# Optimization experiments

Measured on AMD Instinct MI355X. Metric: run time of the kernel, lower is better.

Reference implementation:

```python
import jax, jax.numpy as jnp
import numpy as np

N, M, KNN, KUP, POS_DIM = 15872, 35637, 5, 20, 32


def _pos_emb_table(n, d):
    # transformer-style sinusoidal table (matches PosEmb._define_pos_emb)
    pos = np.arange(n, dtype=np.float32)[:, None]
    i2 = np.arange(0, d, 2, dtype=np.float32)
    div = 10000.0 ** (i2 / d)
    pe = np.zeros((n, d), dtype=np.float32)
    pe[:, 0::2] = np.sin(pos / div)
    pe[:, 1::2] = np.cos(pos / div)
    return jnp.asarray(pe)


def _lrelu(x):
    return jnp.where(x > 0, x, 0.2 * x)


def _gather(x, idx):
    # x: [B,n,d], idx: [B,m,k] -> [B,m,k,d]
    return jax.vmap(lambda xb, ib: xb[ib])(x, idx)


def _knn_idx(x, k):
    # x: [B,n,d]; k nearest excluding self (torch knn drops column 0 of topk)
    xx = jnp.sum(x * x, axis=-1)
    neg = 2.0 * jnp.einsum('bnd,bmd->bnm', x, x) - xx[:, :, None] - xx[:, None, :]
    _, idx = jax.lax.top_k(neg, k + 1)
    return idx[..., 1:]


def _emb_block(feat, idx, ec_w1, ec_s1, ec_h1, ec_w2, ec_b2,
               w1, s1, h1, w2, s2, h2, w3, s3, h3, w4, b4):
    # get_graph_feature: [B,n,k,2*in] = cat(nbr - ctr, ctr)
    nbr = _gather(feat, idx)
    ctr = jnp.broadcast_to(feat[:, :, None, :], nbr.shape)
    e = jnp.concatenate([nbr - ctr, ctr], axis=-1)
    # edge_conv (1x1 conv2d = per-edge linear); BN folded into scale/shift (eval mode)
    e = _lrelu(jnp.einsum('bnkc,oc->bnko', e, ec_w1) * ec_s1 + ec_h1)
    e = jnp.einsum('bnkc,oc->bnko', e, ec_w2) + ec_b2
    f1 = jnp.max(e, axis=2)                                   # max over k neighbors -> [B,n,out]
    fmax = jnp.broadcast_to(jnp.max(f1, axis=1, keepdims=True), f1.shape)
    favg = jnp.broadcast_to(jnp.mean(f1, axis=1, keepdims=True), f1.shape)
    h = jnp.concatenate([feat, f1, fmax, favg], axis=-1)      # [B,n,3*out+in]
    # fc_out: 1x1 conv1d stack = per-point MLP with folded BN + LeakyReLU
    h = _lrelu(h @ w1.T * s1 + h1)
    h = _lrelu(h @ w2.T * s2 + h2)
    h = _lrelu(h @ w3.T * s3 + h3)
    return h @ w4.T + b4


def _forward(lx, ldx, pos_emb,
             b0_ec_w1, b0_ec_s1, b0_ec_h1, b0_ec_w2, b0_ec_b2,
             b0_fc_w1, b0_fc_s1, b0_fc_h1, b0_fc_w2, b0_fc_s2, b0_fc_h2,
             b0_fc_w3, b0_fc_s3, b0_fc_h3, b0_fc_w4, b0_fc_b4,
             b1_ec_w1, b1_ec_s1, b1_ec_h1, b1_ec_w2, b1_ec_b2,
             b1_fc_w1, b1_fc_s1, b1_fc_h1, b1_fc_w2, b1_fc_s2, b1_fc_h2,
             b1_fc_w3, b1_fc_s3, b1_fc_h3, b1_fc_w4, b1_fc_b4,
             up_inputs, up_w0, up_s0, up_h0, up_w_rest, up_s_rest, up_h_rest, up_wf, up_bf,
             dec_w0, dec_b0, dec_w1, dec_b1, dec_w2, dec_b2, dec_w3, dec_b3,
             dec_w4, dec_b4, dec_wf, dec_bf,
             idx0, up_idx):
    B = ldx.shape[0]
    feat_in = jnp.concatenate([ldx, jnp.broadcast_to(pos_emb[None], (B,) + pos_emb.shape)], axis=-1)  # [B,N,35]
    f0 = _emb_block(feat_in, idx0,
                    b0_ec_w1, b0_ec_s1, b0_ec_h1, b0_ec_w2, b0_ec_b2,
                    b0_fc_w1, b0_fc_s1, b0_fc_h1, b0_fc_w2, b0_fc_s2, b0_fc_h2,
                    b0_fc_w3, b0_fc_s3, b0_fc_h3, b0_fc_w4, b0_fc_b4)   # [B,N,64]
    idx1 = _knn_idx(f0, KNN)                                            # dynamic feature-space KNN
    f1 = _emb_block(f0, idx1,
                    b1_ec_w1, b1_ec_s1, b1_ec_h1, b1_ec_w2, b1_ec_b2,
                    b1_fc_w1, b1_fc_s1, b1_fc_h1, b1_fc_w2, b1_fc_s2, b1_fc_h2,
                    b1_fc_w3, b1_fc_s3, b1_fc_h3, b1_fc_w4, b1_fc_b4)   # [B,N,128]
    x_feat = jnp.concatenate([feat_in, f0, f1], axis=-1)                # [B,N,227]
    # Upscale: SIREN-activated 1x1-conv stack -> softmax interpolation weights over KUP lo-res nbrs
    h = jnp.sin(jnp.einsum('bmkc,oc->bmko', up_inputs[:B], up_w0) * up_s0 + up_h0)
    for i in range(up_w_rest.shape[0]):
        h = jnp.sin(jnp.einsum('bmkc,oc->bmko', h, up_w_rest[i]) * up_s_rest[i] + up_h_rest[i])
    logits = jnp.einsum('bmkc,oc->bmko', h, up_wf) + up_bf              # [B,M,KUP,1]
    w = jax.nn.softmax(logits, axis=2)
    grouped = _gather(x_feat, up_idx)                                   # [B,M,KUP,227]
    z = jnp.sum(w * grouped, axis=2)                                    # [B,M,227]
    # SIREN decoder: dims [227,256,128,64,32,16,3]; zip with 5 mods applies first 5 layers + head
    h = jnp.sin(30.0 * (z @ dec_w0.T + dec_b0))
    h = jnp.sin(h @ dec_w1.T + dec_b1)
    h = jnp.sin(h @ dec_w2.T + dec_b2)
    h = jnp.sin(h @ dec_w3.T + dec_b3)
    h = jnp.sin(h @ dec_w4.T + dec_b4)
    return h @ dec_wf.T + dec_bf                                        # [B,M,3]


def setup_inputs():
    key = jax.random.key(0)
    ks = iter(jax.random.split(key, 100))
    def rn(*s):
        return jax.random.normal(next(ks), s, jnp.float32) * 0.05
    def sc(*s):
        return jax.random.uniform(next(ks), s, jnp.float32, minval=0.5, maxval=1.5)
    inp = {}
    inp['lx'] = jax.random.normal(next(ks), (1, N, 3), jnp.float32)
    inp['ldx'] = jax.random.normal(next(ks), (1, N, 3), jnp.float32)
    inp['pos_emb'] = _pos_emb_table(N, POS_DIM)
    inp['idx0'] = jax.random.randint(next(ks), (1, N, KNN), 0, N - 1)
    # EmbModule 0: in=35, out=64
    inp['b0_ec_w1'], inp['b0_ec_s1'], inp['b0_ec_h1'] = rn(128, 70), sc(128), rn(128)
    inp['b0_ec_w2'], inp['b0_ec_b2'] = rn(64, 128), rn(64)
    inp['b0_fc_w1'], inp['b0_fc_s1'], inp['b0_fc_h1'] = rn(192, 227), sc(192), rn(192)
    inp['b0_fc_w2'], inp['b0_fc_s2'], inp['b0_fc_h2'] = rn(128, 192), sc(128), rn(128)
    inp['b0_fc_w3'], inp['b0_fc_s3'], inp['b0_fc_h3'] = rn(64, 128), sc(64), rn(64)
    inp['b0_fc_w4'], inp['b0_fc_b4'] = rn(64, 64), rn(64)
    # EmbModule 1: in=64, out=128
    inp['b1_ec_w1'], inp['b1_ec_s1'], inp['b1_ec_h1'] = rn(256, 128), sc(256), rn(256)
    inp['b1_ec_w2'], inp['b1_ec_b2'] = rn(128, 256), rn(128)
    inp['b1_fc_w1'], inp['b1_fc_s1'], inp['b1_fc_h1'] = rn(384, 448), sc(384), rn(384)
    inp['b1_fc_w2'], inp['b1_fc_s2'], inp['b1_fc_h2'] = rn(256, 384), sc(256), rn(256)
    inp['b1_fc_w3'], inp['b1_fc_s3'], inp['b1_fc_h3'] = rn(128, 256), sc(128), rn(128)
    inp['b1_fc_w4'], inp['b1_fc_b4'] = rn(128, 128), rn(128)
    inp['up_inputs'] = jax.random.uniform(next(ks), (1, M, KUP, 7), jnp.float32)
    inp['up_idx'] = jax.random.randint(next(ks), (1, M, KUP), 0, N - 1)
    inp['up_w0'], inp['up_s0'], inp['up_h0'] = rn(128, 7), sc(128), rn(128)
    inp['up_w_rest'], inp['up_s_rest'], inp['up_h_rest'] = rn(7, 128, 128), sc(7, 128), rn(7, 128)
    inp['up_wf'], inp['up_bf'] = rn(1, 128), rn(1)
    # SIREN decoder
    dd = [227, 256, 128, 64, 32, 16]
    for i in range(5):
        inp['dec_w%d' % i], inp['dec_b%d' % i] = rn(dd[i + 1], dd[i]), rn(dd[i + 1])
    inp['dec_wf'], inp['dec_bf'] = rn(3, 16), rn(3)
    return inp


def reference(lx, ldx, pos_emb, idx0,
              b0_ec_w1, b0_ec_s1, b0_ec_h1, b0_ec_w2, b0_ec_b2,
              b0_fc_w1, b0_fc_s1, b0_fc_h1, b0_fc_w2, b0_fc_s2, b0_fc_h2,
              b0_fc_w3, b0_fc_s3, b0_fc_h3, b0_fc_w4, b0_fc_b4,
              b1_ec_w1, b1_ec_s1, b1_ec_h1, b1_ec_w2, b1_ec_b2,
              b1_fc_w1, b1_fc_s1, b1_fc_h1, b1_fc_w2, b1_fc_s2, b1_fc_h2,
              b1_fc_w3, b1_fc_s3, b1_fc_h3, b1_fc_w4, b1_fc_b4,
              up_inputs, up_idx, up_w0, up_s0, up_h0,
              up_w_rest, up_s_rest, up_h_rest, up_wf, up_bf,
              dec_w0, dec_b0, dec_w1, dec_b1, dec_w2, dec_b2, dec_w3, dec_b3,
              dec_w4, dec_b4, dec_wf, dec_bf):
    return _forward(lx, ldx, pos_emb,
                    b0_ec_w1, b0_ec_s1, b0_ec_h1, b0_ec_w2, b0_ec_b2,
                    b0_fc_w1, b0_fc_s1, b0_fc_h1, b0_fc_w2, b0_fc_s2, b0_fc_h2,
                    b0_fc_w3, b0_fc_s3, b0_fc_h3, b0_fc_w4, b0_fc_b4,
                    b1_ec_w1, b1_ec_s1, b1_ec_h1, b1_ec_w2, b1_ec_b2,
                    b1_fc_w1, b1_fc_s1, b1_fc_h1, b1_fc_w2, b1_fc_s2, b1_fc_h2,
                    b1_fc_w3, b1_fc_s3, b1_fc_h3, b1_fc_w4, b1_fc_b4,
                    up_inputs, up_w0, up_s0, up_h0, up_w_rest, up_s_rest, up_h_rest, up_wf, up_bf,
                    dec_w0, dec_b0, dec_w1, dec_b1, dec_w2, dec_b2, dec_w3, dec_b3,
                    dec_w4, dec_b4, dec_wf, dec_bf,
                    idx0, up_idx)
```

## Files before the change

kernel.cpp:

```cpp
#include <hip/hip_runtime.h>
#include <hip/hip_bf16.h>
#include <math.h>

#define N_PTS 15872
#define M_PTS 35637
#define KNN_K 5
#define KUP   20
#define UP_ROWS (M_PTS * KUP)
#define NTILE (N_PTS/32)
#define N_EDGE (N_PTS*KNN_K)
#define CDIV(a,b) (((a)+(b)-1)/(b))

typedef __hip_bfloat16 bf16;
typedef unsigned int uint;
typedef unsigned short ushort_t;
__device__ __forceinline__ float b2f(bf16 x){ return __bfloat162float(x); }

__device__ __forceinline__ uint f2bf_bits(float x){
  uint u = __float_as_uint(x);
  return (u + 0x7FFFu + ((u>>16)&1u)) >> 16;
}

__device__ __forceinline__ ushort_t f2h_bits(float x){
  union { _Float16 h; ushort_t u; } c; c.h = (_Float16)x; return c.u;
}

typedef __attribute__((ext_vector_type(8))) short bf16x8;
typedef __attribute__((ext_vector_type(8))) _Float16 f16x8;
typedef __attribute__((ext_vector_type(2))) __fp16 fp16x2_t;
typedef __attribute__((ext_vector_type(16))) float f32x16;
union FragAB { bf16x8 v; uint u[4]; };
union FragB  { bf16x8 v; uint4 q; };
union FragH  { f16x8 v; uint4 q; _Float16 h[8]; };
union Acc16  { f32x16 v; float f[16]; };
union H2U    { fp16x2_t h; uint u; };

#define PSWAP(a,b) { \
  unsigned _ax = (unsigned)__shfl_xor((int)(a), 32, 64); \
  unsigned _bx = (unsigned)__shfl_xor((int)(b), 32, 64); \
  unsigned _na = hb2 ? _bx : (a); \
  unsigned _nb = hb2 ? (b) : _ax; \
  (a) = _na; (b) = _nb; }

__global__ void flag_k(const uint* __restrict__ pos_raw, int* __restrict__ flag){
  if (threadIdx.x == 0 && blockIdx.x == 0)
    flag[0] = (pos_raw[0] == 0x3F800000u) ? 1 : 0;
}

struct CvtTab { const void* src[52]; int start[52]; };
__global__ __launch_bounds__(256) void cvt_all_k(CvtTab tab, float* __restrict__ dst,
                                                 const int* __restrict__ flag, int total){
  int i = blockIdx.x*256 + threadIdx.x;
  if (i >= total) return;
  int s = 0;
#pragma unroll 1
  for (int k = 1; k < 52; k++) if (tab.start[k] <= i) s = k;
  int off = i - tab.start[s];
  float v = flag[0] ? b2f(((const bf16*)tab.src[s])[off]) : ((const float*)tab.src[s])[off];
  dst[i] = v;
}

__global__ void packfrag16_k(const float* __restrict__ w, const float* __restrict__ sr,
                             ushort_t* __restrict__ out, int n){
  int i = blockIdx.x*256 + threadIdx.x;
  if (i >= n) return;
  int j = i & 7;
  int lam = (i >> 3) & 63;
  int fg = i >> 9;
  int t = fg & 3, ks = (fg >> 2) & 1, Q = (fg >> 3) & 3, l = fg >> 5;
  int nn = t*32 + (lam & 31);
  int kk = Q*32 + ks*16 + (lam >> 5)*8 + j;
  float x = w[l*16384 + nn*128 + kk] * sr[l*128 + nn];
  out[i] = f2h_bits(x);
}

__global__ void packw_mfma_k(const float* __restrict__ w, ushort_t* __restrict__ whi,
                             ushort_t* __restrict__ wlo, int N, int K, int Kpad, int total){
  int i = blockIdx.x*256 + threadIdx.x;
  if (i >= total) return;
  int j = i & 7;
  int lane = (i >> 3) & 63;
  int fr = i >> 9;
  int nq = Kpad >> 5;
  int ks = fr & 1;
  int q  = (fr >> 1) % nq;
  int nt = (fr >> 1) / nq;
  int n = nt*32 + (lane & 31);
  int k = q*32 + ks*16 + (lane >> 5)*8 + j;
  float x = (n < N && k < K) ? w[(size_t)n*K + k] : 0.f;
  uint hb = f2bf_bits(x);
  uint lb = f2bf_bits(x - __uint_as_float(hb << 16));
  whi[i] = (ushort_t)hb;
  wlo[i] = (ushort_t)lb;
}

__global__ void packknn_k(const float* __restrict__ xf, const float* __restrict__ nr,
                          ushort_t* __restrict__ ahi, ushort_t* __restrict__ alo,
                          ushort_t* __restrict__ bhi, ushort_t* __restrict__ blo){
  int i = blockIdx.x*256 + threadIdx.x;
  if (i >= NTILE*5*64*8) return;
  int e = i & 7;
  int lane = (i >> 3) & 63;
  int rest = i >> 9;
  int kc = rest % 5, jt = rest / 5;
  int n = jt*32 + (lane & 31);
  int k = kc*16 + (lane >> 5)*8 + e;
  float f = (k < 64) ? xf[(size_t)n*227 + 35 + k] : 0.f;
  float av, bv;
  if (k < 64)      { av = 2.f*f;   bv = f; }
  else if (k == 64){ av = nr[n];   bv = -1.f; }
  else if (k == 65){ av = 1.f;     bv = -nr[n]; }
  else             { av = 0.f;     bv = 0.f; }
  uint ah = f2bf_bits(av); uint al = f2bf_bits(av - __uint_as_float(ah<<16));
  uint bh = f2bf_bits(bv); uint bl = f2bf_bits(bv - __uint_as_float(bh<<16));
  ahi[i] = (ushort_t)ah; alo[i] = (ushort_t)al;
  bhi[i] = (ushort_t)bh; blo[i] = (ushort_t)bl;
}

__global__ void fillmark_k(bf16* __restrict__ out, int n){
  int i = blockIdx.x*256 + threadIdx.x;
  if (i < n) out[i] = __float2bfloat16(12345.0f);
}

template<int EPI, int ACT>
__global__ __launch_bounds__(256) void gemm_k(
    const float* __restrict__ A, int lda,
    const float* __restrict__ W, int ldw,
    const float* __restrict__ scale, const float* __restrict__ shift,
    float gmul, float* __restrict__ C, int ldc,
    int M, int Nout, int K)
{
  __shared__ __align__(16) float As[16][64];
  __shared__ __align__(16) float Ws[16][64];
  const int tid = threadIdx.x;
  const int tx = tid & 15, ty = tid >> 4;
  const int bm = blockIdx.x * 64, bn = blockIdx.y * 64;
  const int ar = tid >> 2, ak = (tid & 3) * 4;
  float acc[4][4] = {};
  for (int k0 = 0; k0 < K; k0 += 16) {
    float a0=0.f,a1=0.f,a2=0.f,a3=0.f;
    int grow = bm + ar;
    if (grow < M) {
      const float* ap = A + (size_t)grow * lda + (k0 + ak);
      int rem = K - (k0 + ak);
      if (rem >= 4) { a0=ap[0]; a1=ap[1]; a2=ap[2]; a3=ap[3]; }
      else { if(rem>0)a0=ap[0]; if(rem>1)a1=ap[1]; if(rem>2)a2=ap[2]; }
    }
    float w0=0.f,w1=0.f,w2=0.f,w3=0.f;
    int gn = bn + ar;
    if (gn < Nout) {
      const float* wp = W + (size_t)gn * ldw + (k0 + ak);
      int rem = K - (k0 + ak);
      if (rem >= 4) { w0=wp[0]; w1=wp[1]; w2=wp[2]; w3=wp[3]; }
      else { if(rem>0)w0=wp[0]; if(rem>1)w1=wp[1]; if(rem>2)w2=wp[2]; }
    }
    __syncthreads();
    As[ak+0][ar]=a0; As[ak+1][ar]=a1; As[ak+2][ar]=a2; As[ak+3][ar]=a3;
    Ws[ak+0][ar]=w0; Ws[ak+1][ar]=w1; Ws[ak+2][ar]=w2; Ws[ak+3][ar]=w3;
    __syncthreads();
#pragma unroll
    for (int kk = 0; kk < 16; kk++) {
      float4 av = *reinterpret_cast<const float4*>(&As[kk][ty*4]);
      float4 wv = *reinterpret_cast<const float4*>(&Ws[kk][tx*4]);
      float aa[4] = {av.x,av.y,av.z,av.w};
      float ww[4] = {wv.x,wv.y,wv.z,wv.w};
#pragma unroll
      for (int i=0;i<4;i++)
#pragma unroll
        for (int j=0;j<4;j++) acc[i][j] += aa[i]*ww[j];
    }
  }
#pragma unroll
  for (int i=0;i<4;i++){
    int m = bm + ty*4 + i;
    if (m >= M) continue;
#pragma unroll
    for (int j=0;j<4;j++){
      int n = bn + tx*4 + j;
      if (n >= Nout) continue;
      float v = acc[i][j];
      if (EPI==0)      v = v * scale[n] + shift[n];
      else if (EPI==1) v = v + shift[n];
      else             v = (v + shift[n]) * gmul;
      if (ACT==1)      v = v > 0.f ? v : 0.2f*v;
      else if (ACT==2) v = sinf(v);
      C[(size_t)m*ldc + n] = v;
    }
  }
}

struct MLayer { int K, N, Kq, Nt, woff, soff, hoff, epi, act; float gmul; };
struct MCfg { MLayer L[6]; };

template<int NL, int OUTMODE>
__global__ __launch_bounds__(256) void mlp_fused_k(
    const float* __restrict__ A0, int lda0, int K0, int M,
    MCfg cfg,
    const ushort_t* __restrict__ wh, const ushort_t* __restrict__ wl,
    const float* __restrict__ wc,
    float* __restrict__ Cout, int ldc,
    void* __restrict__ oflg, const int* __restrict__ flag)
{
  __shared__ __align__(16) uint slab[64*256];
  const int tid = threadIdx.x;
  const int lane = tid & 63;
  const int wv = tid >> 6;
  const int np = lane & 31;
  const int hb2 = lane >> 5;
  const int rhalf = wv & 1, thalf = wv >> 1;
  const int rb = blockIdx.x * 64;
  const int row_l = rhalf*32 + np;

  for (int e = tid; e < 64*64; e += 256) {
    int r = e >> 6, g = e & 63;
    int gr = rb + r;
    uint p[4];
#pragma unroll
    for (int u=0;u<4;u++){
      int k = g*4+u;
      float f = (gr < M && k < K0) ? A0[(size_t)gr*lda0 + k] : 0.f;
      uint hb = f2bf_bits(f);
      uint lb = f2bf_bits(f - __uint_as_float(hb<<16));
      p[u] = (hb<<16) | lb;
    }
    *(uint4*)&slab[r*256 + (((g ^ r) & 63)<<2)] = make_uint4(p[0],p[1],p[2],p[3]);
  }
  __syncthreads();

#pragma unroll 1
  for (int l = 0; l < NL; l++){
    const int N = cfg.L[l].N, Kq = cfg.L[l].Kq, Nt = cfg.L[l].Nt;
    const int woff = cfg.L[l].woff, soff = cfg.L[l].soff, hoff = cfg.L[l].hoff;
    const int epi = cfg.L[l].epi, actf = cfg.L[l].act;
    const float gmul = cfg.L[l].gmul;
    Acc16 acc[4];
#pragma unroll
    for (int u=0;u<4;u++)
#pragma unroll
      for (int i=0;i<16;i++) acc[u].f[i] = 0.f;

#pragma unroll 1
    for (int q = 0; q < Kq; q++){
#pragma unroll
      for (int ks = 0; ks < 2; ks++){
        int g0 = (q*32 + ks*16 + hb2*8) >> 2;
        uint4 a0 = *(const uint4*)&slab[row_l*256 + ((((g0  ) ^ row_l) & 63)<<2)];
        uint4 a1 = *(const uint4*)&slab[row_l*256 + ((((g0+1) ^ row_l) & 63)<<2)];
        uint au[8] = {a0.x,a0.y,a0.z,a0.w,a1.x,a1.y,a1.z,a1.w};
        FragAB ah, al;
#pragma unroll
        for (int p=0;p<4;p++){
          ah.u[p] = (au[2*p]>>16)     | (au[2*p+1] & 0xFFFF0000u);
          al.u[p] = (au[2*p]&0xFFFFu) | (au[2*p+1]<<16);
        }
#pragma unroll
        for (int u=0;u<4;u++){
          int t = thalf + u*2;
          if (t < Nt){
            size_t fb = (size_t)woff + ((size_t)((t*Kq + q)*2 + ks))*512 + (size_t)lane*8;
            FragB bh, bl;
            bh.q = *(const uint4*)(wh + fb);
            bl.q = *(const uint4*)(wl + fb);
            acc[u].v = __builtin_amdgcn_mfma_f32_32x32x16_bf16(ah.v, bh.v, acc[u].v, 0,0,0);
            acc[u].v = __builtin_amdgcn_mfma_f32_32x32x16_bf16(al.v, bh.v, acc[u].v, 0,0,0);
            acc[u].v = __builtin_amdgcn_mfma_f32_32x32x16_bf16(ah.v, bl.v, acc[u].v, 0,0,0);
          }
        }
      }
    }
    __syncthreads();
#pragma unroll
    for (int u=0;u<4;u++){
      int t = thalf + u*2;
      if (t < Nt){
        int col = t*32 + np;
        if (col < N){
          float scv = (epi==0) ? wc[soff+col] : 0.f;
          float shv = wc[hoff+col];
#pragma unroll
          for (int reg=0;reg<16;reg++){
            int r32 = (reg&3) + 8*(reg>>2) + 4*hb2;
            float v = acc[u].f[reg];
            if (epi==0)      v = v*scv + shv;
            else if (epi==1) v = v + shv;
            else             v = (v + shv)*gmul;
            if (actf==1)      v = v > 0.f ? v : 0.2f*v;
            else if (actf==2) v = __sinf(v);
            if (l == NL-1){
              int gr = rb + rhalf*32 + r32;
              if (gr < M){
                if (OUTMODE==0) Cout[(size_t)gr*ldc + col] = v;
                else {
                  if (!(fabsf(v) < 1e30f)) v = 777.0f;
                  size_t oi = (size_t)gr*3 + col;
                  if (flag[0]) ((bf16*)oflg)[oi] = __float2bfloat16(v);
                  else         ((float*)oflg)[oi] = v;
                }
              }
            } else {
              int r = rhalf*32 + r32;
              uint hb = f2bf_bits(v);
              uint lb = f2bf_bits(v - __uint_as_float(hb<<16));
              slab[r*256 + ((((col>>2) ^ r) & 63)<<2) + (col&3)] = (hb<<16) | lb;
            }
          }
        }
      }
    }
    __syncthreads();
  }
}

#define INS5(tv, tj, v, j) \
  if ((v) > tv[4]){ tv[4]=(v); tj[4]=(j); \
    _Pragma("unroll") \
    for (int q=4;q>0;q--) \
      if (tv[q] > tv[q-1]){ float tf=tv[q-1]; tv[q-1]=tv[q]; tv[q]=tf; \
                            int ti=tj[q-1]; tj[q-1]=tj[q]; tj[q]=ti; } }

__global__ __launch_bounds__(256) void knn_mfma_k(
    const ushort_t* __restrict__ ahi, const ushort_t* __restrict__ alo,
    const ushort_t* __restrict__ bhi, const ushort_t* __restrict__ blo,
    int* __restrict__ out)
{
  __shared__ float mv[4][32][5];
  __shared__ int   mjj[4][32][5];
  const int tid = threadIdx.x;
  const int lane = tid & 63;
  const int wv = tid >> 6;
  const int np = lane & 31;
  const int hb2 = lane >> 5;
  const int it = blockIdx.x;
  const int ig = it*32 + np;

  FragB vh[5], vl[5];
  {
    size_t bb = (size_t)(it*5)*512 + (size_t)lane*8;
#pragma unroll
    for (int kc=0;kc<5;kc++){
      vh[kc].q = *(const uint4*)(bhi + bb + kc*512);
      vl[kc].q = *(const uint4*)(blo + bb + kc*512);
    }
  }

  float tv[5] = {-1e30f,-1e30f,-1e30f,-1e30f,-1e30f};
  int   tj[5] = {0,0,0,0,0};

  FragB uh[5], ul[5], nh[5], nl[5];
  {
    size_t ab = (size_t)(wv*5)*512 + (size_t)lane*8;
#pragma unroll
    for (int kc=0;kc<5;kc++){
      uh[kc].q = *(const uint4*)(ahi + ab + kc*512);
      ul[kc].q = *(const uint4*)(alo + ab + kc*512);
    }
  }

#pragma unroll 1
  for (int t = 0; t < NTILE/4; t++){
    int jt = wv + t*4;
    if (t+1 < NTILE/4){
      size_t an = (size_t)((jt+4)*5)*512 + (size_t)lane*8;
#pragma unroll
      for (int kc=0;kc<5;kc++){
        nh[kc].q = *(const uint4*)(ahi + an + kc*512);
        nl[kc].q = *(const uint4*)(alo + an + kc*512);
      }
    }
    Acc16 acc;
#pragma unroll
    for (int q=0;q<16;q++) acc.f[q] = 0.f;
#pragma unroll
    for (int kc=0;kc<5;kc++){
      acc.v = __builtin_amdgcn_mfma_f32_32x32x16_bf16(uh[kc].v, vh[kc].v, acc.v, 0,0,0);
      acc.v = __builtin_amdgcn_mfma_f32_32x32x16_bf16(ul[kc].v, vh[kc].v, acc.v, 0,0,0);
      acc.v = __builtin_amdgcn_mfma_f32_32x32x16_bf16(uh[kc].v, vl[kc].v, acc.v, 0,0,0);
    }
    int jb = jt*32 + 4*hb2;
#pragma unroll
    for (int reg=0;reg<16;reg++){
      int j = jb + (reg&3) + 8*(reg>>2);
      float v = acc.f[reg];
      if (j != ig) { INS5(tv, tj, v, j); }
    }
    if (t+1 < NTILE/4){
#pragma unroll
      for (int kc=0;kc<5;kc++){ uh[kc] = nh[kc]; ul[kc] = nl[kc]; }
    }
  }

#pragma unroll
  for (int s=0;s<5;s++){
    float ov = __shfl_xor(tv[s], 32, 64);
    int   oj = __shfl_xor(tj[s], 32, 64);
    INS5(tv, tj, ov, oj);
  }
  if (hb2 == 0){
#pragma unroll
    for (int s=0;s<5;s++){ mv[wv][np][s] = tv[s]; mjj[wv][np][s] = tj[s]; }
  }
  __syncthreads();
  if (tid < 32){
    float bv[5]; int bj[5];
#pragma unroll
    for (int s=0;s<5;s++){ bv[s] = mv[0][tid][s]; bj[s] = mjj[0][tid][s]; }
#pragma unroll
    for (int w=1;w<4;w++)
#pragma unroll
      for (int s=0;s<5;s++){
        float v = mv[w][tid][s]; int j = mjj[w][tid][s];
        INS5(bv, bj, v, j);
      }
    int gi = it*32 + tid;
#pragma unroll
    for (int s=0;s<5;s++) out[gi*KNN_K + s] = bj[s];
  }
}

__global__ __launch_bounds__(256) void siren_fused_k(
    const void* __restrict__ upin,
    const ushort_t* __restrict__ wf16,
    const float* __restrict__ W0c, const float* __restrict__ S0c, const float* __restrict__ H0c,
    const float* __restrict__ HRc,
    const float* __restrict__ WFc, const float* __restrict__ BFc,
    float* __restrict__ logits, const int* __restrict__ flag)
{
  __shared__ float intile[4*32*8];
  __shared__ __align__(16) float w0s[128*8];
  __shared__ __align__(16) float hrs[7*128];
  __shared__ __align__(16) float wfs[128];
  __shared__ float bfs[1];

  const int tid  = threadIdx.x;
  const int lane = tid & 63;
  const int wv   = tid >> 6;
  const int np   = lane & 31;
  const int hb2  = lane >> 5;
  const int rowbase = blockIdx.x * 128 + wv * 32;
  const int isbf = flag[0];
  float* intw = intile + wv*32*8;

  for (int e = tid; e < 128*7; e += 256){
    int c = e/7, k = e%7;
    w0s[c*8+k] = W0c[e]*S0c[c];
  }
  if (tid < 128) w0s[tid*8+7] = H0c[tid];
  for (int e = tid; e < 7*128; e += 256) hrs[e] = HRc[e];
  if (tid < 128) wfs[tid] = WFc[tid];
  if (tid == 0) bfs[0] = BFc[0];
  for (int e = lane; e < 32*7; e += 64) {
    int r = e/7, k = e%7;
    int gr = rowbase + r;
    float v = 0.f;
    if (gr < UP_ROWS)
      v = isbf ? b2f(((const bf16*)upin)[(size_t)gr*7+k]) : ((const float*)upin)[(size_t)gr*7+k];
    intw[r*8+k] = v;
  }
  __syncthreads();

  uint st0[16], st1[16];
  {
    float xin[7];
#pragma unroll
    for (int k=0;k<7;k++) xin[k] = intw[np*8+k];
#pragma unroll
    for (int g = 0; g < 16; g++){
      float xs[4];
#pragma unroll
      for (int j = 0; j < 4; j++){
        int c = g*8 + hb2*4 + j;
        const float4 wa = *(const float4*)&w0s[c*8];
        const float4 wb = *(const float4*)&w0s[c*8+4];
        float a = wb.w;
        a += xin[0]*wa.x; a += xin[1]*wa.y; a += xin[2]*wa.z; a += xin[3]*wa.w;
        a += xin[4]*wb.x; a += xin[5]*wb.y; a += xin[6]*wb.z;
        xs[j] = __sinf(a);
      }
      H2U u0,u1;
      u0.h = __builtin_amdgcn_cvt_pkrtz(xs[0],xs[1]);
      u1.h = __builtin_amdgcn_cvt_pkrtz(xs[2],xs[3]);
      st0[g] = u0.u; st1[g] = u1.u;
    }
  }

  FragH fr[8];
#pragma unroll
  for (int m = 0; m < 8; m++){
    uint a0 = st0[2*m], b0 = st0[2*m+1];
    uint a1 = st1[2*m], b1 = st1[2*m+1];
    PSWAP(a0,b0); PSWAP(a1,b1);
    fr[m].q = make_uint4(a0, a1, b0, b1);
  }

  uint nst0[16], nst1[16];
#pragma unroll 1
  for (int l = 0; l < 7; l++) {
#pragma unroll
    for (int tp = 0; tp < 2; tp++){
      Acc16 acc0, acc1;
#pragma unroll
      for (int i=0;i<16;i++){ acc0.f[i] = 0.f; acc1.f[i] = 0.f; }
#pragma unroll
      for (int m = 0; m < 8; m++){
        int fb = (((l*8 + m)*4 + tp*2) << 9) + lane*8;
        FragH bh0, bh1;
        bh0.q = *(const uint4*)(wf16 + fb);
        bh1.q = *(const uint4*)(wf16 + fb + 512);
        acc0.v = __builtin_amdgcn_mfma_f32_32x32x16_f16(bh0.v, fr[m].v, acc0.v, 0,0,0);
        acc1.v = __builtin_amdgcn_mfma_f32_32x32x16_f16(bh1.v, fr[m].v, acc1.v, 0,0,0);
      }
#pragma unroll
      for (int rg = 0; rg < 4; rg++){
        int g0 = (tp*2+0)*4 + rg;
        const float4 b0v = *(const float4*)&hrs[l*128 + g0*8 + hb2*4];
        float x0 = __sinf(acc0.f[rg*4+0] + b0v.x);
        float x1 = __sinf(acc0.f[rg*4+1] + b0v.y);
        float x2 = __sinf(acc0.f[rg*4+2] + b0v.z);
        float x3 = __sinf(acc0.f[rg*4+3] + b0v.w);
        H2U u0,u1;
        u0.h = __builtin_amdgcn_cvt_pkrtz(x0,x1);
        u1.h = __builtin_amdgcn_cvt_pkrtz(x2,x3);
        nst0[g0] = u0.u; nst1[g0] = u1.u;

        int g1 = (tp*2+1)*4 + rg;
        const float4 b1v = *(const float4*)&hrs[l*128 + g1*8 + hb2*4];
        float y0 = __sinf(acc1.f[rg*4+0] + b1v.x);
        float y1 = __sinf(acc1.f[rg*4+1] + b1v.y);
        float y2 = __sinf(acc1.f[rg*4+2] + b1v.z);
        float y3 = __sinf(acc1.f[rg*4+3] + b1v.w);
        H2U v0,v1;
        v0.h = __builtin_amdgcn_cvt_pkrtz(y0,y1);
        v1.h = __builtin_amdgcn_cvt_pkrtz(y2,y3);
        nst0[g1] = v0.u; nst1[g1] = v1.u;
      }
    }
    if (l < 6){
#pragma unroll
      for (int m = 0; m < 8; m++){
        uint a0 = nst0[2*m], b0 = nst0[2*m+1];
        uint a1 = nst1[2*m], b1 = nst1[2*m+1];
        PSWAP(a0,b0); PSWAP(a1,b1);
        fr[m].q = make_uint4(a0, a1, b0, b1);
      }
    }
  }

  {
    float a = 0.f;
#pragma unroll
    for (int g = 0; g < 16; g++){
      const float4 w4 = *(const float4*)&wfs[g*8 + hb2*4];
      H2U u0,u1; u0.u = nst0[g]; u1.u = nst1[g];
      a += (float)u0.h.x*w4.x + (float)u0.h.y*w4.y
         + (float)u1.h.x*w4.z + (float)u1.h.y*w4.w;
    }
    a += __shfl_xor(a, 32, 64);
    int gr = rowbase + np;
    if (hb2 == 0 && gr < UP_ROWS) logits[gr] = a + bfs[0];
  }
}

__global__ void featin_k(const void* __restrict__ ldx, const void* __restrict__ pos,
                         float* __restrict__ xf, const int* __restrict__ flag){
  int i = blockIdx.x*256 + threadIdx.x;
  if (i >= N_PTS*35) return;
  int n = i / 35, c = i % 35;
  float v;
  if (flag[0]) {
    v = (c < 3) ? b2f(((const bf16*)ldx)[n*3+c]) : b2f(((const bf16*)pos)[n*32 + (c-3)]);
  } else {
    v = (c < 3) ? ((const float*)ldx)[n*3+c] : ((const float*)pos)[n*32 + (c-3)];
  }
  xf[(size_t)n*227 + c] = v;
}

__global__ void gather_e_k(const float* __restrict__ xf, int coff, int CIN,
                           const int* __restrict__ idx, float* __restrict__ e,
                           int n0, int np){
  int W2 = 2*CIN;
  int i = blockIdx.x*256 + threadIdx.x;
  if (i >= np*KNN_K*W2) return;
  int c = i % W2; int ek = i / W2;
  int nl = ek / KNN_K, k = ek % KNN_K;
  int n = n0 + nl;
  int j = idx[n*KNN_K + k];
  float out;
  if (c < CIN) out = xf[(size_t)j*227 + coff + c] - xf[(size_t)n*227 + coff + c];
  else         out = xf[(size_t)n*227 + coff + (c-CIN)];
  e[(size_t)ek*W2 + c] = out;
}

__global__ void kmax_k(const float* __restrict__ e2, int C, float* __restrict__ f1,
                       int n0, int np){
  int i = blockIdx.x*256 + threadIdx.x;
  if (i >= np*C) return;
  int nl = i / C, c = i % C;
  float v = -1e30f;
  for (int k=0;k<KNN_K;k++) v = fmaxf(v, e2[((size_t)nl*KNN_K+k)*C + c]);
  f1[(size_t)(n0+nl)*C + c] = v;
}

template<int C>
__global__ __launch_bounds__(256) void reduce1_k(const float* __restrict__ X, int n,
                                                 float* __restrict__ pmax, float* __restrict__ psum){
  const int tid = threadIdx.x;
  const int c = tid % C;
  const int r0 = tid / C;
  const int TPR = 256 / C;
  float vmax = -1e30f, vsum = 0.f;
  for (int row = blockIdx.x * TPR + r0; row < n; row += gridDim.x * TPR) {
    float v = X[(size_t)row * C + c];
    vmax = fmaxf(vmax, v); vsum += v;
  }
  __shared__ float smax[256], ssum[256];
  smax[tid]=vmax; ssum[tid]=vsum;
  __syncthreads();
  if (tid < C) {
    for (int q=1;q<TPR;q++){ vmax=fmaxf(vmax, smax[q*C+c]); vsum += ssum[q*C+c]; }
    pmax[blockIdx.x*C + c] = vmax; psum[blockIdx.x*C + c] = vsum;
  }
}

template<int C>
__global__ void reduce2_k(const float* __restrict__ pmax, const float* __restrict__ psum,
                          int nblk, float invn, float* __restrict__ fmaxo, float* __restrict__ favgo){
  int c = threadIdx.x; if (c >= C) return;
  float vmax=-1e30f, vsum=0.f;
  for (int b=0;b<nblk;b++){ vmax=fmaxf(vmax,pmax[b*C+c]); vsum+=psum[b*C+c]; }
  fmaxo[c]=vmax; favgo[c]=vsum*invn;
}

__global__ void concat_k(const float* __restrict__ xf, int coff, int CF,
                         const float* __restrict__ f1, int C,
                         const float* __restrict__ fmax, const float* __restrict__ favg,
                         float* __restrict__ h, int n0, int np){
  int W = CF + 3*C;
  int i = blockIdx.x*256 + threadIdx.x;
  if (i >= np*W) return;
  int nl = i / W, c = i % W;
  int n = n0 + nl;
  float v;
  if (c < CF)          v = xf[(size_t)n*227 + coff + c];
  else if (c < CF+C)   v = f1[(size_t)n*C + (c-CF)];
  else if (c < CF+2*C) v = fmax[c-CF-C];
  else                 v = favg[c-CF-2*C];
  h[(size_t)nl*W + c] = v;
}

__global__ void norms_k(const float* __restrict__ xf, float* __restrict__ nr){
  int n = blockIdx.x*256 + threadIdx.x;
  if (n >= N_PTS) return;
  const float* p = xf + (size_t)n*227 + 35;
  float s = 0.f;
  for (int d=0;d<64;d++) s += p[d]*p[d];
  nr[n] = s;
}

__global__ __launch_bounds__(64) void softgather_k(const float* __restrict__ logits,
                                                   const int* __restrict__ up_idx,
                                                   const float* __restrict__ xf,
                                                   float* __restrict__ z){
  __shared__ float lw[KUP]; __shared__ int li[KUP];
  int m = blockIdx.x;
  int tid = threadIdx.x;
  if (tid < KUP){ lw[tid] = logits[(size_t)m*KUP + tid]; li[tid] = up_idx[(size_t)m*KUP + tid]; }
  __syncthreads();
  float mx = -1e30f;
  for (int k=0;k<KUP;k++) mx = fmaxf(mx, lw[k]);
  __syncthreads();
  if (tid < KUP) lw[tid] = expf(lw[tid]-mx);
  __syncthreads();
  float s = 0.f;
  for (int k=0;k<KUP;k++) s += lw[k];
  float inv = 1.f/s;
  for (int c = tid; c < 227; c += 64){
    float acc = 0.f;
    for (int k=0;k<KUP;k++) acc += lw[k] * xf[(size_t)li[k]*227 + c];
    z[(size_t)m*227 + c] = acc*inv;
  }
}

extern "C" void kernel_launch(void* const* d_in, const int* in_sizes, int n_in,
                              void* d_out, int out_size, void* d_ws, size_t ws_size,
                              hipStream_t stream) {
  const int *idx0  = (const int*)d_in[3];
  const int *upidx = (const int*)d_in[37];

  float* ws = (float*)d_ws;
  float* x_feat = ws;
  float* f1b    = ws + 3602944;
  float* pmax   = ws + 5634560;
  float* psum   = ws + 5667328;
  float* fmaxv  = ws + 5700096;
  float* favgv  = ws + 5700224;
  int*   flag   = (int*)(ws + 5700352);
  int*   idx1   = (int*)(ws + 5700368);
  float* nrm    = ws + 5779728;
  float* logits = ws + 5795600;
  float* wcvt   = ws + 6508352;
  float* S      = ws + 7214400;
  ushort_t* whi  = (ushort_t*)(S + 9662464);
  ushort_t* wlo  = whi + 114688;
  ushort_t* gwhi = wlo + 114688;
  ushort_t* gwlo = gwhi + 331776;

  const size_t NEED = (size_t)(7214400 + 9662464) * 4
                    + (size_t)(114688*2 + 331776*2) * 2;
  if (ws_size < NEED) {
    fillmark_k<<<CDIV(out_size,256),256,0,stream>>>((bf16*)d_out, out_size);
    return;
  }

  flag_k<<<1,64,0,stream>>>((const uint*)d_in[2], flag);
  CvtTab tab;
  int wcoff = 0, seg = 0;
  auto CVT = [&](int i, int n)->const float* {
    tab.src[seg] = d_in[i]; tab.start[seg] = wcoff; seg++;
    const float* p = wcvt + wcoff; wcoff += n;
    return p;
  };
  const float *E0W1=CVT(4,8960),  *E0S1=CVT(5,128),  *E0H1=CVT(6,128),
              *E0W2=CVT(7,8192),  *E0B2=CVT(8,64);
  const float *F0W1=CVT(9,43584), *F0S1=CVT(10,192), *F0H1=CVT(11,192),
              *F0W2=CVT(12,24576),*F0S2=CVT(13,128), *F0H2=CVT(14,128),
              *F0W3=CVT(15,8192), *F0S3=CVT(16,64),  *F0H3=CVT(17,64),
              *F0W4=CVT(18,4096), *F0B4=CVT(19,64);
  const float *E1W1=CVT(20,32768),*E1S1=CVT(21,256), *E1H1=CVT(22,256),
              *E1W2=CVT(23,32768),*E1B2=CVT(24,128);
  const float *F1W1=CVT(25,172032),*F1S1=CVT(26,384),*F1H1=CVT(27,384),
              *F1W2=CVT(28,98304),*F1S2=CVT(29,256), *F1H2=CVT(30,256),
              *F1W3=CVT(31,32768),*F1S3=CVT(32,128), *F1H3=CVT(33,128),
              *F1W4=CVT(34,16384),*F1B4=CVT(35,128);
  const float *UPW0=CVT(38,896),  *UPS0=CVT(39,128), *UPH0=CVT(40,128),
              *UPWR=CVT(41,114688),*UPSR=CVT(42,896),*UPHR=CVT(43,896),
              *UPWF=CVT(44,128),  *UPBF=CVT(45,1);
  const float *DW0=CVT(46,58112), *DB0=CVT(47,256),
              *DW1=CVT(48,32768), *DB1=CVT(49,128),
              *DW2=CVT(50,8192),  *DB2=CVT(51,64),
              *DW3=CVT(52,2048),  *DB3=CVT(53,32),
              *DW4=CVT(54,512),   *DB4=CVT(55,16),
              *DWF=CVT(56,48),    *DBF=CVT(57,3);
  cvt_all_k<<<CDIV(wcoff,256),256,0,stream>>>(tab, wcvt, flag, wcoff);

  packfrag16_k<<<CDIV(114688,256),256,0,stream>>>(UPWR, UPSR, whi, 114688);

  int offs[16]; const float* srcs[16]; int Ns[16], Ks[16], Kps[16];
  {
    int o = 0, q = 0;
    auto REG = [&](const float* s, int N, int K, int Kpad){
      srcs[q]=s; Ns[q]=N; Ks[q]=K; Kps[q]=Kpad; offs[q]=o;
      o += CDIV(N,32)*32*Kpad; q++;
    };
    REG(F0W1,192,227,256); REG(F0W2,128,192,192); REG(F0W3,64,128,128); REG(F0W4,64,64,64);
    REG(DW0,256,227,256);  REG(DW1,128,256,256);  REG(DW2,64,128,128);
    REG(DW3,32,64,64);     REG(DW4,16,32,32);     REG(DWF,3,16,32);
    REG(E0W1,128,70,96);   REG(E0W2,64,128,128);
    REG(E1W1,256,128,128); REG(E1W2,128,256,256);
    REG(F1W3,128,256,256); REG(F1W4,128,128,128);
  }
  for (int q = 0; q < 16; q++){
    int total = CDIV(Ns[q],32)*32*Kps[q];
    packw_mfma_k<<<CDIV(total,256),256,0,stream>>>(srcs[q], gwhi+offs[q], gwlo+offs[q],
                                                   Ns[q], Ks[q], Kps[q], total);
  }

  auto OFF = [&](const float* p){ return (int)(p - wcvt); };
  MCfg cfc0{};
  cfc0.L[0] = {227,192,8,6, offs[0], OFF(F0S1), OFF(F0H1), 0,1, 0.f};
  cfc0.L[1] = {192,128,6,4, offs[1], OFF(F0S2), OFF(F0H2), 0,1, 0.f};
  cfc0.L[2] = {128, 64,4,2, offs[2], OFF(F0S3), OFF(F0H3), 0,1, 0.f};
  cfc0.L[3] = { 64, 64,2,2, offs[3], 0,         OFF(F0B4), 1,0, 0.f};
  MCfg cdec{};
  cdec.L[0] = {227,256,8,8, offs[4], 0, OFF(DB0), 2,2, 30.f};
  cdec.L[1] = {256,128,8,4, offs[5], 0, OFF(DB1), 1,2, 0.f};
  cdec.L[2] = {128, 64,4,2, offs[6], 0, OFF(DB2), 1,2, 0.f};
  cdec.L[3] = { 64, 32,2,1, offs[7], 0, OFF(DB3), 1,2, 0.f};
  cdec.L[4] = { 32, 16,1,1, offs[8], 0, OFF(DB4), 1,2, 0.f};
  cdec.L[5] = { 16,  3,1,1, offs[9], 0, OFF(DBF), 1,0, 0.f};
  MCfg ce0{};
  ce0.L[0] = { 70,128,3,4, offs[10], OFF(E0S1), OFF(E0H1), 0,1, 0.f};
  ce0.L[1] = {128, 64,4,2, offs[11], 0,         OFF(E0B2), 1,0, 0.f};
  MCfg ce1{};
  ce1.L[0] = {128,256,4,8, offs[12], OFF(E1S1), OFF(E1H1), 0,1, 0.f};
  ce1.L[1] = {256,128,8,4, offs[13], 0,         OFF(E1B2), 1,0, 0.f};
  MCfg cf1t{};
  cf1t.L[0] = {256,128,8,4, offs[14], OFF(F1S3), OFF(F1H3), 0,1, 0.f};
  cf1t.L[1] = {128,128,4,4, offs[15], 0,         OFF(F1B4), 1,0, 0.f};

  const float invN = 1.f/(float)N_PTS;
  const int CHN = 8192;

  featin_k<<<CDIV(N_PTS*35,256),256,0,stream>>>(d_in[1], d_in[2], x_feat, flag);

  {
    const int P0 = N_PTS/2;
    for (int n0 = 0; n0 < N_PTS; n0 += P0) {
      int ne = P0 * KNN_K;
      float* eA   = S;
      float* eOut = S + 2777600;
      gather_e_k<<<CDIV(ne*70,256),256,0,stream>>>(x_feat, 0, 35, idx0, eA, n0, P0);
      mlp_fused_k<2,0><<<CDIV(ne,64),256,0,stream>>>(
          eA,70,70,ne, ce0, gwhi,gwlo,wcvt, eOut,64, nullptr, flag);
      kmax_k<<<CDIV(P0*64,256),256,0,stream>>>(eOut, 64, f1b, n0, P0);
    }
  }
  reduce1_k<64><<<256,256,0,stream>>>(f1b, N_PTS, pmax, psum);
  reduce2_k<64><<<1,64,0,stream>>>(pmax, psum, 256, invN, fmaxv, favgv);
  {
    float* h = S;
    concat_k<<<CDIV(N_PTS*227,256),256,0,stream>>>(x_feat,0,35, f1b,64, fmaxv,favgv, h, 0, N_PTS);
    mlp_fused_k<4,0><<<CDIV(N_PTS,64),256,0,stream>>>(
        h,227,227,N_PTS, cfc0, gwhi,gwlo,wcvt, x_feat+35,227, nullptr, flag);
  }

  norms_k<<<CDIV(N_PTS,256),256,0,stream>>>(x_feat, nrm);
  {
    const int PLANE = NTILE*5*64*8;
    ushort_t* ajhi = (ushort_t*)S;
    ushort_t* ajlo = ajhi + PLANE;
    ushort_t* bihi = ajlo + PLANE;
    ushort_t* bilo = bihi + PLANE;
    packknn_k<<<CDIV(PLANE,256),256,0,stream>>>(x_feat, nrm, ajhi, ajlo, bihi, bilo);
    knn_mfma_k<<<NTILE,256,0,stream>>>(ajhi, ajlo, bihi, bilo, idx1);
  }

  {
    const int P1 = 5952;
    for (int n0 = 0; n0 < N_PTS; n0 += P1) {
      int np = N_PTS - n0; if (np > P1) np = P1;
      int ne = np * KNN_K;
      float* eA   = S;
      float* eOut = S + 3809280;
      gather_e_k<<<CDIV(ne*128,256),256,0,stream>>>(x_feat, 35, 64, idx1, eA, n0, np);
      mlp_fused_k<2,0><<<CDIV(ne,64),256,0,stream>>>(
          eA,128,128,ne, ce1, gwhi,gwlo,wcvt, eOut,128, nullptr, flag);
      kmax_k<<<CDIV(np*128,256),256,0,stream>>>(eOut, 128, f1b, n0, np);
    }
  }
  reduce1_k<128><<<256,256,0,stream>>>(f1b, N_PTS, pmax, psum);
  reduce2_k<128><<<1,128,0,stream>>>(pmax, psum, 256, invN, fmaxv, favgv);
  for (int n0 = 0; n0 < N_PTS; n0 += CHN) {
    int np = N_PTS - n0; if (np > CHN) np = CHN;
    float* h  = S;
    float* a1 = S + 3670016;
    int gx = CDIV(np,64);
    concat_k<<<CDIV(np*448,256),256,0,stream>>>(x_feat,35,64, f1b,128, fmaxv,favgv, h, n0, np);
    gemm_k<0,1><<<dim3(gx,6),256,0,stream>>>(h,448,  F1W1,448, F1S1,F1H1,0.f, a1,384, np,384,448);
    gemm_k<0,1><<<dim3(gx,4),256,0,stream>>>(a1,384, F1W2,384, F1S2,F1H2,0.f, h,256,  np,256,384);
    mlp_fused_k<2,0><<<gx,256,0,stream>>>(
        h,256,256,np, cf1t, gwhi,gwlo,wcvt, x_feat+(size_t)n0*227+99,227, nullptr, flag);
  }

  siren_fused_k<<<CDIV(UP_ROWS,128),256,0,stream>>>(
      d_in[36], whi, UPW0, UPS0, UPH0, UPHR, UPWF, UPBF, logits, flag);
  float* zbuf = S;
  softgather_k<<<M_PTS,64,0,stream>>>(logits, upidx, x_feat, zbuf);

  mlp_fused_k<6,1><<<CDIV(M_PTS,64),256,0,stream>>>(
      zbuf,227,227,M_PTS, cdec, gwhi,gwlo,wcvt, nullptr,0, d_out, flag);
}
```

Measured before the change: 1.994 ms.

## Fold broadcast global max/avg features into first-layer bias; drop SIREN shuffle swaps

The global max and mean features are identical for every point, so their contribution through the first fc layer is precomputed once per block as a per-output bias (W·v·scale + shift). This shrinks the concat and the first GEMM K dimension from 227 to 99 and from 448 to 192, removing redundant matmul work and memory traffic. It also re-packs the SIREN fp16 weight fragments so the per-layer cross-lane shuffle swaps are no longer needed. The trade-off is extra small kernels and reliance on the new fragment packing being consistent with the MFMA operand layout.

```diff
diff --git a/kernel.cpp b/kernel.cpp
--- a/kernel.cpp
+++ b/kernel.cpp
@@ -35,13 +35,6 @@
 union Acc16  { f32x16 v; float f[16]; };
 union H2U    { fp16x2_t h; uint u; };
 
-#define PSWAP(a,b) { \
-  unsigned _ax = (unsigned)__shfl_xor((int)(a), 32, 64); \
-  unsigned _bx = (unsigned)__shfl_xor((int)(b), 32, 64); \
-  unsigned _na = hb2 ? _bx : (a); \
-  unsigned _nb = hb2 ? (b) : _ax; \
-  (a) = _na; (b) = _nb; }
-
 __global__ void flag_k(const uint* __restrict__ pos_raw, int* __restrict__ flag){
   if (threadIdx.x == 0 && blockIdx.x == 0)
     flag[0] = (pos_raw[0] == 0x3F800000u) ? 1 : 0;
@@ -69,13 +62,14 @@
   int fg = i >> 9;
   int t = fg & 3, ks = (fg >> 2) & 1, Q = (fg >> 3) & 3, l = fg >> 5;
   int nn = t*32 + (lam & 31);
-  int kk = Q*32 + ks*16 + (lam >> 5)*8 + j;
+  int kk = Q*32 + ks*16 + ((j>>2)<<3) + ((lam>>5)<<2) + (j&3);
   float x = w[l*16384 + nn*128 + kk] * sr[l*128 + nn];
   out[i] = f2h_bits(x);
 }
 
 __global__ void packw_mfma_k(const float* __restrict__ w, ushort_t* __restrict__ whi,
-                             ushort_t* __restrict__ wlo, int N, int K, int Kpad, int total){
+                             ushort_t* __restrict__ wlo, int N, int K, int ldk,
+                             int Kpad, int total){
   int i = blockIdx.x*256 + threadIdx.x;
   if (i >= total) return;
   int j = i & 7;
@@ -87,7 +81,7 @@
   int nt = (fr >> 1) / nq;
   int n = nt*32 + (lane & 31);
   int k = q*32 + ks*16 + (lane >> 5)*8 + j;
-  float x = (n < N && k < K) ? w[(size_t)n*K + k] : 0.f;
+  float x = (n < N && k < K) ? w[(size_t)n*ldk + k] : 0.f;
   uint hb = f2bf_bits(x);
   uint lb = f2bf_bits(x - __uint_as_float(hb << 16));
   whi[i] = (ushort_t)hb;
@@ -120,6 +114,20 @@
 __global__ void fillmark_k(bf16* __restrict__ out, int n){
   int i = blockIdx.x*256 + threadIdx.x;
   if (i < n) out[i] = __float2bfloat16(12345.0f);
+}
+
+__global__ void foldshift_k(const float* __restrict__ W, int ldw,
+                            int off1, int C1, const float* __restrict__ v1,
+                            int off2, int C2, const float* __restrict__ v2,
+                            const float* __restrict__ scale, const float* __restrict__ shift,
+                            float* __restrict__ out, int N){
+  int n = blockIdx.x*256 + threadIdx.x;
+  if (n >= N) return;
+  const float* wr = W + (size_t)n*ldw;
+  float s = 0.f;
+  for (int j=0;j<C1;j++) s += wr[off1+j]*v1[j];
+  for (int j=0;j<C2;j++) s += wr[off2+j]*v2[j];
+  out[n] = s*scale[n] + shift[n];
 }
 
 template<int EPI, int ACT>
@@ -485,12 +493,8 @@
 
   FragH fr[8];
 #pragma unroll
-  for (int m = 0; m < 8; m++){
-    uint a0 = st0[2*m], b0 = st0[2*m+1];
-    uint a1 = st1[2*m], b1 = st1[2*m+1];
-    PSWAP(a0,b0); PSWAP(a1,b1);
-    fr[m].q = make_uint4(a0, a1, b0, b1);
-  }
+  for (int m = 0; m < 8; m++)
+    fr[m].q = make_uint4(st0[2*m], st1[2*m], st0[2*m+1], st1[2*m+1]);
 
   uint nst0[16], nst1[16];
 #pragma unroll 1
@@ -536,12 +540,8 @@
     }
     if (l < 6){
 #pragma unroll
-      for (int m = 0; m < 8; m++){
-        uint a0 = nst0[2*m], b0 = nst0[2*m+1];
-        uint a1 = nst1[2*m], b1 = nst1[2*m+1];
-        PSWAP(a0,b0); PSWAP(a1,b1);
-        fr[m].q = make_uint4(a0, a1, b0, b1);
-      }
+      for (int m = 0; m < 8; m++)
+        fr[m].q = make_uint4(nst0[2*m], nst1[2*m], nst0[2*m+1], nst1[2*m+1]);
     }
   }
 
@@ -644,6 +644,18 @@
   else if (c < CF+C)   v = f1[(size_t)n*C + (c-CF)];
   else if (c < CF+2*C) v = fmax[c-CF-C];
   else                 v = favg[c-CF-2*C];
+  h[(size_t)nl*W + c] = v;
+}
+
+__global__ void concat2_k(const float* __restrict__ xf, int coff, int CF,
+                          const float* __restrict__ f1, int C,
+                          float* __restrict__ h, int n0, int np){
+  int W = CF + C;
+  int i = blockIdx.x*256 + threadIdx.x;
+  if (i >= np*W) return;
+  int nl = i / W, c = i % W;
+  int n = n0 + nl;
+  float v = (c < CF) ? xf[(size_t)n*227 + coff + c] : f1[(size_t)n*C + (c-CF)];
   h[(size_t)nl*W + c] = v;
 }
 
@@ -699,6 +711,8 @@
   float* logits = ws + 5795600;
   float* wcvt   = ws + 6508352;
   float* S      = ws + 7214400;
+  float* fold0  = S + 9500000;
+  float* fold1  = S + 9500192;
   ushort_t* whi  = (ushort_t*)(S + 9662464);
   ushort_t* wlo  = whi + 114688;
   ushort_t* gwhi = wlo + 114688;
@@ -744,29 +758,31 @@
 
   packfrag16_k<<<CDIV(114688,256),256,0,stream>>>(UPWR, UPSR, whi, 114688);
 
-  int offs[16]; const float* srcs[16]; int Ns[16], Ks[16], Kps[16];
+  int offs[16]; const float* srcs[16]; int Ns[16], Ks[16], Ldk[16], Kps[16];
   {
     int o = 0, q = 0;
-    auto REG = [&](const float* s, int N, int K, int Kpad){
-      srcs[q]=s; Ns[q]=N; Ks[q]=K; Kps[q]=Kpad; offs[q]=o;
+    auto REG = [&](const float* s, int N, int K, int ldk, int Kpad){
+      srcs[q]=s; Ns[q]=N; Ks[q]=K; Ldk[q]=ldk; Kps[q]=Kpad; offs[q]=o;
       o += CDIV(N,32)*32*Kpad; q++;
     };
-    REG(F0W1,192,227,256); REG(F0W2,128,192,192); REG(F0W3,64,128,128); REG(F0W4,64,64,64);
-    REG(DW0,256,227,256);  REG(DW1,128,256,256);  REG(DW2,64,128,128);
-    REG(DW3,32,64,64);     REG(DW4,16,32,32);     REG(DWF,3,16,32);
-    REG(E0W1,128,70,96);   REG(E0W2,64,128,128);
-    REG(E1W1,256,128,128); REG(E1W2,128,256,256);
-    REG(F1W3,128,256,256); REG(F1W4,128,128,128);
+    REG(F0W1,192, 99,227,128);
+    REG(F0W2,128,192,192,192); REG(F0W3,64,128,128,128); REG(F0W4,64,64,64,64);
+    REG(DW0,256,227,227,256);  REG(DW1,128,256,256,256);  REG(DW2,64,128,128,128);
+    REG(DW3,32,64,64,64);      REG(DW4,16,32,32,32);      REG(DWF,3,16,16,32);
+    REG(E0W1,128,70,70,96);    REG(E0W2,64,128,128,128);
+    REG(E1W1,256,128,128,128); REG(E1W2,128,256,256,256);
+    REG(F1W3,128,256,256,256); REG(F1W4,128,128,128,128);
   }
   for (int q = 0; q < 16; q++){
     int total = CDIV(Ns[q],32)*32*Kps[q];
     packw_mfma_k<<<CDIV(total,256),256,0,stream>>>(srcs[q], gwhi+offs[q], gwlo+offs[q],
-                                                   Ns[q], Ks[q], Kps[q], total);
+                                                   Ns[q], Ks[q], Ldk[q], Kps[q], total);
   }
 
   auto OFF = [&](const float* p){ return (int)(p - wcvt); };
+  const int HOFF0 = (int)(fold0 - wcvt);
   MCfg cfc0{};
-  cfc0.L[0] = {227,192,8,6, offs[0], OFF(F0S1), OFF(F0H1), 0,1, 0.f};
+  cfc0.L[0] = { 99,192,4,6, offs[0], OFF(F0S1), HOFF0,     0,1, 0.f};
   cfc0.L[1] = {192,128,6,4, offs[1], OFF(F0S2), OFF(F0H2), 0,1, 0.f};
   cfc0.L[2] = {128, 64,4,2, offs[2], OFF(F0S3), OFF(F0H3), 0,1, 0.f};
   cfc0.L[3] = { 64, 64,2,2, offs[3], 0,         OFF(F0B4), 1,0, 0.f};
@@ -806,11 +822,13 @@
   }
   reduce1_k<64><<<256,256,0,stream>>>(f1b, N_PTS, pmax, psum);
   reduce2_k<64><<<1,64,0,stream>>>(pmax, psum, 256, invN, fmaxv, favgv);
+  foldshift_k<<<1,256,0,stream>>>(F0W1,227, 99,64,fmaxv, 163,64,favgv,
+                                  F0S1,F0H1, fold0, 192);
   {
     float* h = S;
-    concat_k<<<CDIV(N_PTS*227,256),256,0,stream>>>(x_feat,0,35, f1b,64, fmaxv,favgv, h, 0, N_PTS);
+    concat2_k<<<CDIV(N_PTS*99,256),256,0,stream>>>(x_feat,0,35, f1b,64, h, 0, N_PTS);
     mlp_fused_k<4,0><<<CDIV(N_PTS,64),256,0,stream>>>(
-        h,227,227,N_PTS, cfc0, gwhi,gwlo,wcvt, x_feat+35,227, nullptr, flag);
+        h,99,99,N_PTS, cfc0, gwhi,gwlo,wcvt, x_feat+35,227, nullptr, flag);
   }
 
   norms_k<<<CDIV(N_PTS,256),256,0,stream>>>(x_feat, nrm);
@@ -839,13 +857,15 @@
   }
   reduce1_k<128><<<256,256,0,stream>>>(f1b, N_PTS, pmax, psum);
   reduce2_k<128><<<1,128,0,stream>>>(pmax, psum, 256, invN, fmaxv, favgv);
+  foldshift_k<<<2,256,0,stream>>>(F1W1,448, 192,128,fmaxv, 320,128,favgv,
+                                  F1S1,F1H1, fold1, 384);
   for (int n0 = 0; n0 < N_PTS; n0 += CHN) {
     int np = N_PTS - n0; if (np > CHN) np = CHN;
     float* h  = S;
     float* a1 = S + 3670016;
     int gx = CDIV(np,64);
-    concat_k<<<CDIV(np*448,256),256,0,stream>>>(x_feat,35,64, f1b,128, fmaxv,favgv, h, n0, np);
-    gemm_k<0,1><<<dim3(gx,6),256,0,stream>>>(h,448,  F1W1,448, F1S1,F1H1,0.f, a1,384, np,384,448);
+    concat2_k<<<CDIV(np*192,256),256,0,stream>>>(x_feat,35,64, f1b,128, h, n0, np);
+    gemm_k<0,1><<<dim3(gx,6),256,0,stream>>>(h,192,  F1W1,448, F1S1,fold1,0.f, a1,384, np,384,192);
     gemm_k<0,1><<<dim3(gx,4),256,0,stream>>>(a1,384, F1W2,384, F1S2,F1H2,0.f, h,256,  np,256,384);
     mlp_fused_k<2,0><<<gx,256,0,stream>>>(
         h,256,256,np, cf1t, gwhi,gwlo,wcvt, x_feat+(size_t)n0*227+99,227, nullptr, flag);
```

New measurement: 2.045 ms. 1.03x slower.
